# Performance work log

Hardware: AMD Instinct MI355X
Metric: run time of the kernel (lower is better)

The kernel has to match this reference:

```python
import jax, jax.numpy as jnp
import numpy as np

EPS = 1e-6  # flax LayerNorm default

def layer_norm(x, scale, bias):
    mean = jnp.mean(x, axis=-1, keepdims=True)
    var = jnp.mean(jnp.square(x - mean), axis=-1, keepdims=True)
    return (x - mean) * jax.lax.rsqrt(var + EPS) * scale + bias

def setup_inputs() -> dict:
    key = jax.random.key(0)
    ks = jax.random.split(key, 8)
    B, M, D, R, H = 8, 8192, 512, 64, 128
    s = 0.02
    return {
        "memory": jax.random.normal(ks[0], (B, M, D), dtype=jnp.float32),
        "output_tokens": jax.random.normal(ks[1], (B, R, D), dtype=jnp.float32),
        # erase path params
        "ln_e_scale": jnp.ones((D,), jnp.float32),
        "ln_e_bias": jnp.zeros((D,), jnp.float32),
        "We1": jax.random.normal(ks[2], (D, H), dtype=jnp.float32) * s,
        "be1": jnp.zeros((H,), jnp.float32),
        "We2": jax.random.normal(ks[3], (H, R), dtype=jnp.float32) * s,
        "be2": jnp.zeros((R,), jnp.float32),
        # add path params
        "ln_a_scale": jnp.ones((D,), jnp.float32),
        "ln_a_bias": jnp.zeros((D,), jnp.float32),
        "Wa1": jax.random.normal(ks[4], (D, H), dtype=jnp.float32) * s,
        "ba1": jnp.zeros((H,), jnp.float32),
        "Wa2": jax.random.normal(ks[5], (H, D), dtype=jnp.float32) * s,
        "ba2": jnp.zeros((D,), jnp.float32),
    }

def reference(memory, output_tokens, ln_e_scale, ln_e_bias, We1, be1, We2, be2,
              ln_a_scale, ln_a_bias, Wa1, ba1, Wa2, ba2):
    # Erase weights: LN -> Dense(H) -> gelu -> Dense(r) -> transpose -> softmax over m
    e = layer_norm(memory, ln_e_scale, ln_e_bias)                  # [b,m,d]
    e = jax.nn.gelu(e @ We1 + be1)                                 # [b,m,H] (tanh approx, flax default)
    e = e @ We2 + be2                                              # [b,m,r]
    erase = jax.nn.softmax(jnp.transpose(e, (0, 2, 1)), axis=-1)   # [b,r,m], softmax over m
    # Add vectors: LN -> Dense(H) -> gelu -> Dense(d)
    a = layer_norm(output_tokens, ln_a_scale, ln_a_bias)           # [b,r,d]
    a = jax.nn.gelu(a @ Wa1 + ba1)                                 # [b,r,H]
    add = a @ Wa2 + ba2                                            # [b,r,d]
    # sum_r erase[b,r,m]*add[b,r,d] -> [b,m,d]; source builds a [b,r,m,d]
    # intermediate; this einsum is the identical math, fused as a batched matmul.
    ea = jnp.einsum('brm,brd->bmd', erase, add)
    # new_memory = memory * (1 - ea) + ea   (erase then add, add_matrix == ea)
    return memory * (1.0 - ea) + ea
```

## Files before the change

### kernel.cpp

```cpp
#include <hip/hip_runtime.h>
#include <hip/hip_bf16.h>
#include <math.h>

#define BB 8
#define MM 8192
#define DD 512
#define RR 64
#define HH 128

typedef __attribute__((ext_vector_type(8))) short bf16x8;
typedef __attribute__((ext_vector_type(4))) short bf16x4;
typedef __attribute__((ext_vector_type(4))) float f32x4;

#define XN_LD 520
#define H_LD  136

__device__ __forceinline__ float gelu_tanh(float x) {
    float u = 0.7978845608028654f * (x + 0.044715f * x * x * x);
    float e = __expf(2.0f * u);
    float t = 1.0f - 2.0f / (e + 1.0f);
    return 0.5f * x * (1.0f + t);
}

__device__ __forceinline__ short f2bf(float f) {
    unsigned int u = __float_as_uint(f);
    unsigned int r = u + 0x7FFFu + ((u >> 16) & 1u);
    return (short)(r >> 16);
}

__global__ __launch_bounds__(256) void prep_weights_kernel(
    const float* __restrict__ We1, const float* __restrict__ We2,
    short* __restrict__ We1T, short* __restrict__ We2T)
{
    int idx = blockIdx.x * 256 + threadIdx.x;
    if (idx < 128 * 512) {
        int n = idx >> 9, k = idx & 511;
        We1T[idx] = f2bf(We1[k * HH + n]);
    } else {
        int j = idx - 128 * 512;
        if (j < 64 * 128) {
            int n = j >> 7, k = j & 127;
            We2T[j] = f2bf(We2[k * RR + n]);
        }
    }
}

__global__ __launch_bounds__(256) void add_path_kernel(
    const float* __restrict__ ot, const float* __restrict__ scale,
    const float* __restrict__ bias, const float* __restrict__ Wa1,
    const float* __restrict__ ba1, const float* __restrict__ Wa2,
    const float* __restrict__ ba2, float* __restrict__ add_out)
{
    int tid = threadIdx.x;
    int b = blockIdx.x >> 6, r = blockIdx.x & 63;
    const float* x = ot + (size_t)(b * RR + r) * DD;
    __shared__ float xs[DD];
    __shared__ float hsm[HH];
    __shared__ float hpart[HH];
    __shared__ float rs[4], rq[4];
    float v0 = x[tid], v1 = x[tid + 256];
    float s = v0 + v1, q = v0 * v0 + v1 * v1;
    #pragma unroll
    for (int off = 32; off > 0; off >>= 1) { s += __shfl_xor(s, off); q += __shfl_xor(q, off); }
    if ((tid & 63) == 0) { rs[tid >> 6] = s; rq[tid >> 6] = q; }
    __syncthreads();
    s = rs[0] + rs[1] + rs[2] + rs[3];
    q = rq[0] + rq[1] + rq[2] + rq[3];
    float mean = s * (1.0f / DD);
    float var = q * (1.0f / DD) - mean * mean;
    float inv = rsqrtf(var + 1e-6f);
    xs[tid]       = (v0 - mean) * inv * scale[tid]       + bias[tid];
    xs[tid + 256] = (v1 - mean) * inv * scale[tid + 256] + bias[tid + 256];
    __syncthreads();
    {
        int col = tid & 127, part = tid >> 7;
        float acc = part ? 0.0f : ba1[col];
        const float* wp = Wa1 + (size_t)(part * 256) * HH + col;
        const float* xp = xs + part * 256;
        #pragma unroll 4
        for (int k = 0; k < 256; k++) acc = fmaf(xp[k], wp[(size_t)k * HH], acc);
        if (part) hpart[col] = acc;
        __syncthreads();
        if (!part) hsm[col] = gelu_tanh(acc + hpart[col]);
    }
    __syncthreads();
    int d0 = tid, d1 = tid + 256;
    float a0 = ba2[d0], a1 = ba2[d1];
    #pragma unroll 4
    for (int k = 0; k < HH; k++) {
        float hk = hsm[k];
        a0 = fmaf(hk, Wa2[k * DD + d0], a0);
        a1 = fmaf(hk, Wa2[k * DD + d1], a1);
    }
    add_out[(size_t)(b * RR + r) * DD + d0] = a0;
    add_out[(size_t)(b * RR + r) * DD + d1] = a1;
}

__global__ __launch_bounds__(512) void erase_mfma_kernel(
    const float* __restrict__ mem, const float* __restrict__ scale,
    const float* __restrict__ bias, const short* __restrict__ We1T,
    const float* __restrict__ be1, const short* __restrict__ We2T,
    const float* __restrict__ be2, short* __restrict__ logits_bf,
    float* __restrict__ psum)
{
    __shared__ short xn[32 * XN_LD];
    short* hsm = xn;

    int tid = threadIdx.x;
    int b = blockIdx.x >> 6;
    int cbase = (blockIdx.x & 63) * 4;

    int w = tid >> 6, l = tid & 63;
    int lr = l & 15, g = l >> 4, kg = g * 8;
    int row = tid >> 4, sub = tid & 15;
    int mhalf = w & 1, nf2 = w >> 1;

    const short* bp0 = We1T + ((size_t)(w * 16 + lr) << 9) + kg;
    bf16x8 bfr[16];
    #pragma unroll
    for (int ks = 0; ks < 16; ks++) bfr[ks] = *(const bf16x8*)(bp0 + ks * 32);
    const short* bp2 = We2T + (nf2 * 16 + lr) * 128 + kg;
    bf16x8 bfr2[4];
    #pragma unroll
    for (int ks = 0; ks < 4; ks++) bfr2[ks] = *(const bf16x8*)(bp2 + ks * 32);

    const float4* scv = (const float4*)scale;
    const float4* biv = (const float4*)bias;

    float4 v[8];
    {
        const float4* srcv = (const float4*)(mem + (size_t)(b * MM + cbase * 32 + row) * DD);
        #pragma unroll
        for (int j = 0; j < 8; j++) v[j] = srcv[j * 16 + sub];
    }

    for (int c = 0; c < 4; c++) {
        int m0 = (cbase + c) * 32;

        {
            float s = 0.f, q = 0.f;
            #pragma unroll
            for (int j = 0; j < 8; j++) {
                s += v[j].x + v[j].y + v[j].z + v[j].w;
                q += v[j].x*v[j].x + v[j].y*v[j].y + v[j].z*v[j].z + v[j].w*v[j].w;
            }
            #pragma unroll
            for (int off = 1; off <= 8; off <<= 1) { s += __shfl_xor(s, off); q += __shfl_xor(q, off); }
            float mean = s * (1.0f / 512.0f);
            float var = q * (1.0f / 512.0f) - mean * mean;
            float inv = rsqrtf(var + 1e-6f);
            #pragma unroll
            for (int j = 0; j < 8; j++) {
                float4 sc = scv[j * 16 + sub], bi = biv[j * 16 + sub];
                bf16x4 o;
                o[0] = f2bf((v[j].x - mean) * inv * sc.x + bi.x);
                o[1] = f2bf((v[j].y - mean) * inv * sc.y + bi.y);
                o[2] = f2bf((v[j].z - mean) * inv * sc.z + bi.z);
                o[3] = f2bf((v[j].w - mean) * inv * sc.w + bi.w);
                *(bf16x4*)&xn[row * XN_LD + (j * 16 + sub) * 4] = o;
            }
        }
        __syncthreads();

        if (c < 3) {
            const float4* srcv = (const float4*)(mem + (size_t)(b * MM + m0 + 32 + row) * DD);
            #pragma unroll
            for (int j = 0; j < 8; j++) v[j] = srcv[j * 16 + sub];
        }

        f32x4 acc0 = {0.f,0.f,0.f,0.f}, acc1 = acc0;
        #pragma unroll
        for (int ks = 0; ks < 16; ks++) {
            int k0 = ks * 32;
            bf16x8 a0 = *(const bf16x8*)&xn[lr * XN_LD + k0 + kg];
            bf16x8 a1 = *(const bf16x8*)&xn[(16 + lr) * XN_LD + k0 + kg];
            acc0 = __builtin_amdgcn_mfma_f32_16x16x32_bf16(a0, bfr[ks], acc0, 0, 0, 0);
            acc1 = __builtin_amdgcn_mfma_f32_16x16x32_bf16(a1, bfr[ks], acc1, 0, 0, 0);
        }
        __syncthreads();
        {
            int col = w * 16 + lr;
            float bv = be1[col];
            #pragma unroll
            for (int rg = 0; rg < 4; rg++) {
                hsm[(g * 4 + rg) * H_LD + col]      = f2bf(gelu_tanh(acc0[rg] + bv));
                hsm[(16 + g * 4 + rg) * H_LD + col] = f2bf(gelu_tanh(acc1[rg] + bv));
            }
        }
        __syncthreads();

        f32x4 c0 = {0.f,0.f,0.f,0.f};
        #pragma unroll
        for (int ks = 0; ks < 4; ks++) {
            bf16x8 a2 = *(const bf16x8*)&hsm[(mhalf * 16 + lr) * H_LD + ks * 32 + kg];
            c0 = __builtin_amdgcn_mfma_f32_16x16x32_bf16(a2, bfr2[ks], c0, 0, 0, 0);
        }
        {
            int cc = nf2 * 16 + lr;
            float bv = be2[cc];
            float sm = 0.f;
            #pragma unroll
            for (int rg = 0; rg < 4; rg++) {
                float ev = __expf(c0[rg] + bv);
                sm += ev;
                logits_bf[(size_t)(b * MM + m0 + mhalf * 16 + g * 4 + rg) * 64 + cc] = f2bf(ev);
            }
            sm += __shfl_xor(sm, 16);
            sm += __shfl_xor(sm, 32);
            if (l < 16) {
                int ch2 = (m0 >> 4) + mhalf;
                psum[((size_t)b * 512 + ch2) * 64 + cc] = sm;
            }
        }
        __syncthreads();
    }
}

__global__ __launch_bounds__(256) void softmax_finalize_kernel(
    const float* __restrict__ psum, const float* __restrict__ add,
    float* __restrict__ rinv, short* __restrict__ addT)
{
    int b = blockIdx.x;
    int g = threadIdx.x >> 6, r = threadIdx.x & 63;
    __shared__ float sm_[4][64];
    __shared__ float rinvl[64];
    float sm = 0.0f;
    for (int ch = g; ch < 512; ch += 4)
        sm += psum[((size_t)b * 512 + ch) * 64 + r];
    sm_[g][r] = sm;
    __syncthreads();
    if (threadIdx.x < 64) {
        float S = sm_[0][threadIdx.x] + sm_[1][threadIdx.x]
                + sm_[2][threadIdx.x] + sm_[3][threadIdx.x];
        float rv = 1.0f / S;
        rinv[b * 64 + threadIdx.x] = rv;
        rinvl[threadIdx.x] = rv;
    }
    __syncthreads();
    const float* addb = add + (size_t)b * RR * DD;
    #pragma unroll 8
    for (int i = 0; i < 128; i++) {
        int idx = threadIdx.x + i * 256;
        int d = idx >> 6, rr = idx & 63;
        addT[(size_t)b * 32768 + idx] = f2bf(addb[(size_t)rr * 512 + d] * rinvl[rr]);
    }
}

__global__ __launch_bounds__(256, 4) void apply_mfma_kernel(
    const float* __restrict__ mem, const short* __restrict__ logits_bf,
    const short* __restrict__ addT, float* __restrict__ out)
{
    int tid = threadIdx.x;
    int w = tid >> 6, l = tid & 63;
    int b = blockIdx.x >> 8;
    int mt = blockIdx.x & 255;
    int m0 = mt * 32;
    int lr = l & 15, kg = (l >> 4) * 8;
    int nbase = w * 128;
    const short* aT = addT + (size_t)b * 512 * 64;

    for (int ms = 0; ms < 2; ms++) {
        float mv[8][4];
        #pragma unroll
        for (int nf = 0; nf < 8; nf++) {
            int d = nbase + nf * 16 + lr;
            #pragma unroll
            for (int rg = 0; rg < 4; rg++) {
                int m = m0 + ms * 16 + (l >> 4) * 4 + rg;
                mv[nf][rg] = mem[(size_t)(b * MM + m) * DD + d];
            }
        }
        int mrow = m0 + ms * 16 + lr;
        const short* lp = logits_bf + (size_t)(b * MM + mrow) * 64 + kg;
        bf16x8 a0 = *(const bf16x8*)lp;
        bf16x8 a1 = *(const bf16x8*)(lp + 32);

        f32x4 acc[8];
        #pragma unroll
        for (int nf = 0; nf < 8; nf++) {
            int d = nbase + nf * 16 + lr;
            bf16x8 b0 = *(const bf16x8*)&aT[d * 64 + kg];
            bf16x8 b1 = *(const bf16x8*)&aT[d * 64 + 32 + kg];
            f32x4 c = (f32x4){0.f, 0.f, 0.f, 0.f};
            c = __builtin_amdgcn_mfma_f32_16x16x32_bf16(a0, b0, c, 0, 0, 0);
            c = __builtin_amdgcn_mfma_f32_16x16x32_bf16(a1, b1, c, 0, 0, 0);
            acc[nf] = c;
        }
        #pragma unroll
        for (int nf = 0; nf < 8; nf++) {
            int d = nbase + nf * 16 + lr;
            #pragma unroll
            for (int rg = 0; rg < 4; rg++) {
                int m = m0 + ms * 16 + (l >> 4) * 4 + rg;
                size_t off = (size_t)(b * MM + m) * DD + d;
                float mvv = mv[nf][rg];
                out[off] = fmaf(acc[nf][rg], 1.0f - mvv, mvv);
            }
        }
    }
}

extern "C" void kernel_launch(void* const* d_in, const int* in_sizes, int n_in,
                              void* d_out, int out_size, void* d_ws, size_t ws_size,
                              hipStream_t stream) {
    const float* memory = (const float*)d_in[0];
    const float* ot     = (const float*)d_in[1];
    const float* ln_e_s = (const float*)d_in[2];
    const float* ln_e_b = (const float*)d_in[3];
    const float* We1    = (const float*)d_in[4];
    const float* be1    = (const float*)d_in[5];
    const float* We2    = (const float*)d_in[6];
    const float* be2    = (const float*)d_in[7];
    const float* ln_a_s = (const float*)d_in[8];
    const float* ln_a_b = (const float*)d_in[9];
    const float* Wa1    = (const float*)d_in[10];
    const float* ba1    = (const float*)d_in[11];
    const float* Wa2    = (const float*)d_in[12];
    const float* ba2    = (const float*)d_in[13];
    float* out = (float*)d_out;

    float* ws        = (float*)d_ws;
    float* add_ws    = ws;
    short* logits_bf = (short*)(ws + 262144);
    float* psumw     = (float*)(logits_bf + 4194304);
    float* rinvw     = psumw + 262144;
    short* We1T      = (short*)(rinvw + 512);
    short* We2T      = We1T + 128 * 512;
    short* addT      = We2T + 64 * 128;

    hipLaunchKernelGGL(prep_weights_kernel, dim3(288), dim3(256), 0, stream,
                       We1, We2, We1T, We2T);
    hipLaunchKernelGGL(add_path_kernel, dim3(BB * RR), dim3(256), 0, stream,
                       ot, ln_a_s, ln_a_b, Wa1, ba1, Wa2, ba2, add_ws);
    hipLaunchKernelGGL(erase_mfma_kernel, dim3(BB * 64), dim3(512), 0, stream,
                       memory, ln_e_s, ln_e_b, We1T, be1, We2T, be2, logits_bf, psumw);
    hipLaunchKernelGGL(softmax_finalize_kernel, dim3(BB), dim3(256), 0, stream,
                       psumw, add_ws, rinvw, addT);
    hipLaunchKernelGGL(apply_mfma_kernel, dim3(BB * 256), dim3(256), 0, stream,
                       memory, logits_bf, addT, out);
}
```

Before: 206.8 us.

## Make erase kernel wave-independent, one 16-row chunk per wave without block syncs

Replaces the 512-thread block erase kernel, which shared a 32-row LDS tile and used several block barriers, with a kernel in which each wave handles 16 memory rows on its own. Each wave reads its rows straight from global memory in MFMA fragment layout, twice (once for the LN statistics, once to normalize), and builds its bf16 A operands in registers. Weight fragments are loaded from global or cache inside the MFMA loop, and LDS is used only per wave for the hidden activations. This is meant to remove block-level syncs and raise parallelism. In exchange, the memory tensor is read twice per row, global loads are strided per lane, and each wave reloads all weight fragments.

```diff
diff --git a/kernel.cpp b/kernel.cpp
--- a/kernel.cpp
+++ b/kernel.cpp
@@ -12,7 +12,6 @@
 typedef __attribute__((ext_vector_type(4))) short bf16x4;
 typedef __attribute__((ext_vector_type(4))) float f32x4;
 
-#define XN_LD 520
 #define H_LD  136
 
 __device__ __forceinline__ float gelu_tanh(float x) {
@@ -96,123 +95,107 @@
     add_out[(size_t)(b * RR + r) * DD + d1] = a1;
 }
 
-__global__ __launch_bounds__(512) void erase_mfma_kernel(
+__global__ __launch_bounds__(256) void erase_wave_kernel(
     const float* __restrict__ mem, const float* __restrict__ scale,
     const float* __restrict__ bias, const short* __restrict__ We1T,
     const float* __restrict__ be1, const short* __restrict__ We2T,
     const float* __restrict__ be2, short* __restrict__ logits_bf,
     float* __restrict__ psum)
 {
-    __shared__ short xn[32 * XN_LD];
-    short* hsm = xn;
+    __shared__ short hs_all[4][16 * H_LD];
 
     int tid = threadIdx.x;
-    int b = blockIdx.x >> 6;
-    int cbase = (blockIdx.x & 63) * 4;
-
     int w = tid >> 6, l = tid & 63;
     int lr = l & 15, g = l >> 4, kg = g * 8;
-    int row = tid >> 4, sub = tid & 15;
-    int mhalf = w & 1, nf2 = w >> 1;
-
-    const short* bp0 = We1T + ((size_t)(w * 16 + lr) << 9) + kg;
-    bf16x8 bfr[16];
-    #pragma unroll
-    for (int ks = 0; ks < 16; ks++) bfr[ks] = *(const bf16x8*)(bp0 + ks * 32);
-    const short* bp2 = We2T + (nf2 * 16 + lr) * 128 + kg;
-    bf16x8 bfr2[4];
-    #pragma unroll
-    for (int ks = 0; ks < 4; ks++) bfr2[ks] = *(const bf16x8*)(bp2 + ks * 32);
-
-    const float4* scv = (const float4*)scale;
-    const float4* biv = (const float4*)bias;
-
-    float4 v[8];
-    {
-        const float4* srcv = (const float4*)(mem + (size_t)(b * MM + cbase * 32 + row) * DD);
-        #pragma unroll
-        for (int j = 0; j < 8; j++) v[j] = srcv[j * 16 + sub];
-    }
-
-    for (int c = 0; c < 4; c++) {
-        int m0 = (cbase + c) * 32;
-
-        {
-            float s = 0.f, q = 0.f;
-            #pragma unroll
-            for (int j = 0; j < 8; j++) {
-                s += v[j].x + v[j].y + v[j].z + v[j].w;
-                q += v[j].x*v[j].x + v[j].y*v[j].y + v[j].z*v[j].z + v[j].w*v[j].w;
-            }
-            #pragma unroll
-            for (int off = 1; off <= 8; off <<= 1) { s += __shfl_xor(s, off); q += __shfl_xor(q, off); }
-            float mean = s * (1.0f / 512.0f);
-            float var = q * (1.0f / 512.0f) - mean * mean;
-            float inv = rsqrtf(var + 1e-6f);
-            #pragma unroll
-            for (int j = 0; j < 8; j++) {
-                float4 sc = scv[j * 16 + sub], bi = biv[j * 16 + sub];
-                bf16x4 o;
-                o[0] = f2bf((v[j].x - mean) * inv * sc.x + bi.x);
-                o[1] = f2bf((v[j].y - mean) * inv * sc.y + bi.y);
-                o[2] = f2bf((v[j].z - mean) * inv * sc.z + bi.z);
-                o[3] = f2bf((v[j].w - mean) * inv * sc.w + bi.w);
-                *(bf16x4*)&xn[row * XN_LD + (j * 16 + sub) * 4] = o;
-            }
-        }
-        __syncthreads();
-
-        if (c < 3) {
-            const float4* srcv = (const float4*)(mem + (size_t)(b * MM + m0 + 32 + row) * DD);
-            #pragma unroll
-            for (int j = 0; j < 8; j++) v[j] = srcv[j * 16 + sub];
-        }
-
-        f32x4 acc0 = {0.f,0.f,0.f,0.f}, acc1 = acc0;
-        #pragma unroll
-        for (int ks = 0; ks < 16; ks++) {
-            int k0 = ks * 32;
-            bf16x8 a0 = *(const bf16x8*)&xn[lr * XN_LD + k0 + kg];
-            bf16x8 a1 = *(const bf16x8*)&xn[(16 + lr) * XN_LD + k0 + kg];
-            acc0 = __builtin_amdgcn_mfma_f32_16x16x32_bf16(a0, bfr[ks], acc0, 0, 0, 0);
-            acc1 = __builtin_amdgcn_mfma_f32_16x16x32_bf16(a1, bfr[ks], acc1, 0, 0, 0);
-        }
-        __syncthreads();
-        {
-            int col = w * 16 + lr;
-            float bv = be1[col];
-            #pragma unroll
-            for (int rg = 0; rg < 4; rg++) {
-                hsm[(g * 4 + rg) * H_LD + col]      = f2bf(gelu_tanh(acc0[rg] + bv));
-                hsm[(16 + g * 4 + rg) * H_LD + col] = f2bf(gelu_tanh(acc1[rg] + bv));
-            }
-        }
-        __syncthreads();
-
-        f32x4 c0 = {0.f,0.f,0.f,0.f};
-        #pragma unroll
-        for (int ks = 0; ks < 4; ks++) {
-            bf16x8 a2 = *(const bf16x8*)&hsm[(mhalf * 16 + lr) * H_LD + ks * 32 + kg];
-            c0 = __builtin_amdgcn_mfma_f32_16x16x32_bf16(a2, bfr2[ks], c0, 0, 0, 0);
-        }
-        {
-            int cc = nf2 * 16 + lr;
-            float bv = be2[cc];
-            float sm = 0.f;
-            #pragma unroll
-            for (int rg = 0; rg < 4; rg++) {
-                float ev = __expf(c0[rg] + bv);
-                sm += ev;
-                logits_bf[(size_t)(b * MM + m0 + mhalf * 16 + g * 4 + rg) * 64 + cc] = f2bf(ev);
-            }
-            sm += __shfl_xor(sm, 16);
-            sm += __shfl_xor(sm, 32);
-            if (l < 16) {
-                int ch2 = (m0 >> 4) + mhalf;
-                psum[((size_t)b * 512 + ch2) * 64 + cc] = sm;
-            }
-        }
-        __syncthreads();
+    int gw = blockIdx.x * 4 + w;
+    int b = gw >> 9;
+    int chunk = gw & 511;
+    int m0 = chunk * 16;
+    short* hsm = hs_all[w];
+
+    const float* rowp = mem + (size_t)(b * MM + m0 + lr) * DD + kg;
+
+    float s = 0.f, q = 0.f;
+    #pragma unroll 4
+    for (int ks = 0; ks < 16; ks++) {
+        float4 u0 = *(const float4*)(rowp + ks * 32);
+        float4 u1 = *(const float4*)(rowp + ks * 32 + 4);
+        s += u0.x + u0.y + u0.z + u0.w + u1.x + u1.y + u1.z + u1.w;
+        q += u0.x*u0.x + u0.y*u0.y + u0.z*u0.z + u0.w*u0.w
+           + u1.x*u1.x + u1.y*u1.y + u1.z*u1.z + u1.w*u1.w;
+    }
+    s += __shfl_xor(s, 16); q += __shfl_xor(q, 16);
+    s += __shfl_xor(s, 32); q += __shfl_xor(q, 32);
+    float mean = s * (1.0f / 512.0f);
+    float var = q * (1.0f / 512.0f) - mean * mean;
+    float inv = rsqrtf(var + 1e-6f);
+
+    const float* scp = scale + kg;
+    const float* bip = bias + kg;
+    f32x4 acc[8];
+    #pragma unroll
+    for (int nf = 0; nf < 8; nf++) acc[nf] = (f32x4){0.f, 0.f, 0.f, 0.f};
+    #pragma unroll 4
+    for (int ks = 0; ks < 16; ks++) {
+        float4 u0 = *(const float4*)(rowp + ks * 32);
+        float4 u1 = *(const float4*)(rowp + ks * 32 + 4);
+        float4 sc0 = *(const float4*)(scp + ks * 32);
+        float4 sc1 = *(const float4*)(scp + ks * 32 + 4);
+        float4 bi0 = *(const float4*)(bip + ks * 32);
+        float4 bi1 = *(const float4*)(bip + ks * 32 + 4);
+        bf16x8 a;
+        a[0] = f2bf((u0.x - mean) * inv * sc0.x + bi0.x);
+        a[1] = f2bf((u0.y - mean) * inv * sc0.y + bi0.y);
+        a[2] = f2bf((u0.z - mean) * inv * sc0.z + bi0.z);
+        a[3] = f2bf((u0.w - mean) * inv * sc0.w + bi0.w);
+        a[4] = f2bf((u1.x - mean) * inv * sc1.x + bi1.x);
+        a[5] = f2bf((u1.y - mean) * inv * sc1.y + bi1.y);
+        a[6] = f2bf((u1.z - mean) * inv * sc1.z + bi1.z);
+        a[7] = f2bf((u1.w - mean) * inv * sc1.w + bi1.w);
+        #pragma unroll
+        for (int nf = 0; nf < 8; nf++) {
+            bf16x8 bf = *(const bf16x8*)(We1T + (size_t)(nf * 16 + lr) * 512 + ks * 32 + kg);
+            acc[nf] = __builtin_amdgcn_mfma_f32_16x16x32_bf16(a, bf, acc[nf], 0, 0, 0);
+        }
+    }
+
+    #pragma unroll
+    for (int nf = 0; nf < 8; nf++) {
+        int col = nf * 16 + lr;
+        float bv = be1[col];
+        #pragma unroll
+        for (int rg = 0; rg < 4; rg++)
+            hsm[(g * 4 + rg) * H_LD + col] = f2bf(gelu_tanh(acc[nf][rg] + bv));
+    }
+
+    f32x4 c2[4];
+    #pragma unroll
+    for (int nf = 0; nf < 4; nf++) c2[nf] = (f32x4){0.f, 0.f, 0.f, 0.f};
+    #pragma unroll
+    for (int ks = 0; ks < 4; ks++) {
+        bf16x8 a2 = *(const bf16x8*)&hsm[lr * H_LD + ks * 32 + kg];
+        #pragma unroll
+        for (int nf = 0; nf < 4; nf++) {
+            bf16x8 bf = *(const bf16x8*)(We2T + (nf * 16 + lr) * 128 + ks * 32 + kg);
+            c2[nf] = __builtin_amdgcn_mfma_f32_16x16x32_bf16(a2, bf, c2[nf], 0, 0, 0);
+        }
+    }
+
+    #pragma unroll
+    for (int nf = 0; nf < 4; nf++) {
+        int c = nf * 16 + lr;
+        float bv = be2[c];
+        float sm = 0.f;
+        #pragma unroll
+        for (int rg = 0; rg < 4; rg++) {
+            float ev = __expf(c2[nf][rg] + bv);
+            sm += ev;
+            logits_bf[(size_t)(b * MM + m0 + g * 4 + rg) * 64 + c] = f2bf(ev);
+        }
+        sm += __shfl_xor(sm, 16);
+        sm += __shfl_xor(sm, 32);
+        if (g == 0)
+            psum[((size_t)b * 512 + chunk) * 64 + c] = sm;
     }
 }
 
@@ -332,7 +315,7 @@
                        We1, We2, We1T, We2T);
     hipLaunchKernelGGL(add_path_kernel, dim3(BB * RR), dim3(256), 0, stream,
                        ot, ln_a_s, ln_a_b, Wa1, ba1, Wa2, ba2, add_ws);
-    hipLaunchKernelGGL(erase_mfma_kernel, dim3(BB * 64), dim3(512), 0, stream,
+    hipLaunchKernelGGL(erase_wave_kernel, dim3(BB * 512 / 4), dim3(256), 0, stream,
                        memory, ln_e_s, ln_e_b, We1T, be1, We2T, be2, logits_bf, psumw);
     hipLaunchKernelGGL(softmax_finalize_kernel, dim3(BB), dim3(256), 0, stream,
                        psumw, add_ws, rinvw, addT);
```

Result: slower. 268.4 us (+29.8%).
